# Kernel tuning notes

Measured on AMD Instinct MI355X. Metric: run time of the kernel, lower is better.

Reference implementation:

```python
import jax, jax.numpy as jnp
import numpy as np

B, T, D = 2, 1024, 1024
H, DK, DV = 16, 64, 128   # head_dim=64, head_v_dim=128 (expand_v=2)
F_HID, CONV = 2816, 4
EPS = 1e-6


def rmsnorm(x, w, eps=EPS):
    return x * jax.lax.rsqrt(jnp.mean(x * x, -1, keepdims=True) + eps) * w


def l2norm(x, eps=1e-6):
    return x * jax.lax.rsqrt(jnp.sum(x * x, -1, keepdims=True) + eps)


def short_conv(x, w):
    # causal depthwise conv1d (kernel CONV, no bias) + silu; x: [B,T,C], w: [C,K]
    K = w.shape[1]
    xp = jnp.pad(x, ((0, 0), (K - 1, 0), (0, 0)))
    y = jax.lax.conv_general_dilated(
        xp, w.T[:, None, :], (1,), 'VALID',
        dimension_numbers=('NWC', 'WIO', 'NWC'), feature_group_count=w.shape[0])
    return jax.nn.silu(y)


def gated_delta_rule(q, k, v, g, beta):
    # q,k: [B,T,H,DK], v: [B,T,H,DV], g,beta: [B,T,H]
    scale = q.shape[-1] ** -0.5
    q = l2norm(q) * scale
    k = l2norm(k)

    def step(S, inp):
        qt, kt, vt, gt, bt = inp          # S: [B,H,DK,DV]
        S = S * jnp.exp(gt)[..., None, None]
        err = jnp.einsum('bhk,bhkv->bhv', kt, S)
        vt = (vt - err) * bt[..., None]
        S = S + kt[..., :, None] * vt[..., None, :]
        ot = jnp.einsum('bhk,bhkv->bhv', qt, S)
        return S, ot

    S0 = jnp.zeros((q.shape[0], H, DK, DV), q.dtype)
    inputs = tuple(jnp.moveaxis(a, 1, 0) for a in (q, k, v, g, beta))
    _, o = jax.lax.scan(step, S0, inputs)
    return jnp.moveaxis(o, 0, 1)  # [B,T,H,DV]


def setup_inputs():
    key = jax.random.key(0)
    ks = jax.random.split(key, 20)
    w = lambda k, shape, s=0.02: jax.random.normal(k, shape, jnp.float32) * s
    return {
        'x': jax.random.normal(ks[0], (B, T, D), jnp.float32),
        'norm1_w': jnp.ones((D,), jnp.float32),
        'norm2_w': jnp.ones((D,), jnp.float32),
        'Wq': w(ks[1], (D, H * DK)),
        'Wk': w(ks[2], (D, H * DK)),
        'Wv': w(ks[3], (D, H * DV)),
        'conv_q': w(ks[4], (H * DK, CONV), 0.3),
        'conv_k': w(ks[5], (H * DK, CONV), 0.3),
        'conv_v': w(ks[6], (H * DV, CONV), 0.3),
        'Wa': w(ks[7], (D, H)),
        'Wb': w(ks[8], (D, H)),
        'dt_bias': jnp.log(jnp.expm1(jax.random.uniform(ks[9], (H,), minval=0.001, maxval=0.1))),
        'A_log': jnp.log(jax.random.uniform(ks[10], (H,), minval=1.0, maxval=16.0)),
        'Wg': w(ks[11], (D, H * DV)),
        'o_norm_w': jnp.ones((DV,), jnp.float32),
        'Wo': w(ks[12], (H * DV, D)),
        'W1': w(ks[13], (D, F_HID)),
        'W3': w(ks[14], (D, F_HID)),
        'W2': w(ks[15], (F_HID, D)),
    }


def reference(x, norm1_w, norm2_w, Wq, Wk, Wv, conv_q, conv_k, conv_v,
              Wa, Wb, dt_bias, A_log, Wg, o_norm_w, Wo, W1, W3, W2):
    # --- pre-norm + GatedDeltaNet ---
    h = rmsnorm(x, norm1_w)
    q = short_conv(h @ Wq, conv_q).reshape(B, T, H, DK)
    k = short_conv(h @ Wk, conv_k).reshape(B, T, H, DK)
    v = short_conv(h @ Wv, conv_v).reshape(B, T, H, DV)
    beta = jax.nn.sigmoid(h @ Wb)                                  # [B,T,H]
    g = -jnp.exp(A_log) * jax.nn.softplus(h @ Wa + dt_bias)       # [B,T,H] decay log
    o = gated_delta_rule(q, k, v, g, beta)                         # [B,T,H,DV]
    gate = (h @ Wg).reshape(B, T, H, DV)
    o = rmsnorm(o, o_norm_w, 1e-5) * jax.nn.silu(gate)             # gated RMSNorm
    x = x + o.reshape(B, T, H * DV) @ Wo                           # residual 1
    # --- pre-norm + SwiGLU FFN ---
    h2 = rmsnorm(x, norm2_w)
    ffn = (jax.nn.silu(h2 @ W1) * (h2 @ W3)) @ W2
    return x + ffn
```

## Files before the change

kernel.cpp:

```cpp
#include <hip/hip_runtime.h>
#include <hip/hip_bf16.h>
#include <math.h>

#define B_  2
#define T_  1024
#define D_  1024
#define H_  16
#define DK_ 64
#define DV_ 128
#define FH_ 2816
#define M_  (B_ * T_)
#define C_  64
#define NCH (T_ / C_)

typedef __attribute__((ext_vector_type(8))) short bf16x8;
typedef __attribute__((ext_vector_type(4))) float f32x4;

__global__ __launch_bounds__(256) void rmsnorm_k(
    const float* __restrict__ x, const float* __restrict__ w,
    float* __restrict__ outf, __hip_bfloat16* __restrict__ outb,
    int D, float eps) {
  const int row = blockIdx.x;
  const float* xr = x + (size_t)row * D;
  float ss = 0.f;
  for (int i = threadIdx.x; i < D; i += blockDim.x) { float v = xr[i]; ss += v * v; }
  for (int off = 32; off > 0; off >>= 1) ss += __shfl_xor(ss, off, 64);
  __shared__ float wsum[4];
  __shared__ float s_scale;
  const int lane = threadIdx.x & 63, wid = threadIdx.x >> 6;
  if (lane == 0) wsum[wid] = ss;
  __syncthreads();
  if (threadIdx.x == 0) {
    float tot = 0.f;
    const int nw = blockDim.x >> 6;
    for (int i = 0; i < nw; ++i) tot += wsum[i];
    s_scale = rsqrtf(tot / (float)D + eps);
  }
  __syncthreads();
  const float sc = s_scale;
  for (int i = threadIdx.x; i < D; i += blockDim.x) {
    const float v = xr[i] * sc * w[i];
    if (outf) outf[(size_t)row * D + i] = v;
    if (outb) outb[(size_t)row * D + i] = __float2bfloat16(v);
  }
}

__global__ __launch_bounds__(256) void transpose_bf16_k(
    const float* __restrict__ W, __hip_bfloat16* __restrict__ Wt, int K, int N) {
  __shared__ float t[32][33];
  const int k0 = blockIdx.y * 32, n0 = blockIdx.x * 32;
  const int c = threadIdx.x & 31, r = threadIdx.x >> 5;
#pragma unroll
  for (int i = 0; i < 4; ++i)
    t[r + 8 * i][c] = W[(size_t)(k0 + r + 8 * i) * N + n0 + c];
  __syncthreads();
#pragma unroll
  for (int i = 0; i < 4; ++i)
    Wt[(size_t)(n0 + r + 8 * i) * K + k0 + c] = __float2bfloat16(t[c][r + 8 * i]);
}

__device__ __forceinline__ void gload_lds16(const void* g, void* l) {
  __builtin_amdgcn_global_load_lds(
      (const __attribute__((address_space(1))) void*)g,
      (__attribute__((address_space(3))) void*)l, 16, 0, 0);
}

template<int BM, int BN>
__global__ __launch_bounds__(256) void mfma_gemm_k(
    const __hip_bfloat16* __restrict__ A, const __hip_bfloat16* __restrict__ Bt,
    const float* __restrict__ res, void* __restrict__ Cout,
    int M, int N, int K, int mode) {
  __shared__ __hip_bfloat16 As[2][BM * 32];
  __shared__ __hip_bfloat16 Bs[2][BN * 32];
  constexpr int MF = BM / 32;
  constexpr int NF = BN / 32;
  const int tid = threadIdx.x;
  const int lane = tid & 63;
  const int wv = tid >> 6;
  const int wm = (wv >> 1) * (BM / 2), wn = (wv & 1) * (BN / 2);
  const int bm = blockIdx.y * BM, bn = blockIdx.x * BN;
  const int l15 = lane & 15, lq8 = (lane >> 4) * 8;
  const int ar = tid >> 2;
  const int ac = (tid & 3) * 8;
  const size_t Abase = (size_t)(bm + ar) * K + ac;
  const size_t Bbase = (size_t)(bn + ar) * K + ac;
  f32x4 acc[MF][NF];
#pragma unroll
  for (int i = 0; i < MF; ++i)
#pragma unroll
    for (int j = 0; j < NF; ++j) acc[i][j] = (f32x4){0.f, 0.f, 0.f, 0.f};

  auto stage = [&](int buf, int k0) {
    gload_lds16(A + Abase + k0, (char*)&As[buf][0] + tid * 16);
    if constexpr (BM == 128)
      gload_lds16(A + Abase + (size_t)64 * K + k0,
                  (char*)&As[buf][0] + tid * 16 + 4096);
    gload_lds16(Bt + Bbase + k0, (char*)&Bs[buf][0] + tid * 16);
    if constexpr (BN == 128)
      gload_lds16(Bt + Bbase + (size_t)64 * K + k0,
                  (char*)&Bs[buf][0] + tid * 16 + 4096);
  };

  stage(0, 0);
  __syncthreads();
  int cur = 0;
#pragma unroll 2
  for (int k0 = 0; k0 < K; k0 += 32) {
    if (k0 + 32 < K) stage(cur ^ 1, k0 + 32);
    bf16x8 af[MF], bfr[NF];
#pragma unroll
    for (int i = 0; i < MF; ++i)
      af[i] = *(const bf16x8*)(&As[cur][0] + (wm + i * 16 + l15) * 32 + lq8);
#pragma unroll
    for (int j = 0; j < NF; ++j)
      bfr[j] = *(const bf16x8*)(&Bs[cur][0] + (wn + j * 16 + l15) * 32 + lq8);
#pragma unroll
    for (int i = 0; i < MF; ++i)
#pragma unroll
      for (int j = 0; j < NF; ++j)
        acc[i][j] = __builtin_amdgcn_mfma_f32_16x16x32_bf16(af[i], bfr[j], acc[i][j], 0, 0, 0);
    __syncthreads();
    cur ^= 1;
  }
  const int r0 = (lane >> 4) * 4;
#pragma unroll
  for (int i = 0; i < MF; ++i) {
#pragma unroll
    for (int j = 0; j < NF; ++j) {
      const int row = bm + wm + i * 16 + r0;
      const int col = bn + wn + j * 16 + l15;
#pragma unroll
      for (int r = 0; r < 4; ++r) {
        const size_t idx = (size_t)(row + r) * N + col;
        const float a = acc[i][j][r];
        if (mode == 0) ((float*)Cout)[idx] = a;
        else if (mode == 1) ((float*)Cout)[idx] = a + res[idx];
        else {
          const float s = res[idx];
          ((__hip_bfloat16*)Cout)[idx] =
              __float2bfloat16(s * (1.f / (1.f + __expf(-s))) * a);
        }
      }
    }
  }
}

__global__ __launch_bounds__(256) void skinny_k(
    const float* __restrict__ h, const float* __restrict__ Wa,
    const float* __restrict__ Wb, float* __restrict__ pa,
    float* __restrict__ pb, int K) {
  __shared__ float hl[D_];
  __shared__ float red[8][32];
  const int row = blockIdx.x;
  const int tid = threadIdx.x;
  {
    const float4* src = (const float4*)(h + (size_t)row * K);
    ((float4*)hl)[tid] = src[tid];
  }
  __syncthreads();
  const int col = tid & 31, sub = tid >> 5;
  const float* W = (col < 16) ? Wa : Wb;
  const int cc = col & 15;
  float s = 0.f;
  const int kk0 = sub * 128;
  for (int k = kk0; k < kk0 + 128; ++k) s += hl[k] * W[k * H_ + cc];
  red[sub][col] = s;
  __syncthreads();
  if (tid < 32) {
    float t = 0.f;
#pragma unroll
    for (int i = 0; i < 8; ++i) t += red[i][tid];
    if (tid < 16) pa[(size_t)row * H_ + tid] = t;
    else          pb[(size_t)row * H_ + tid - 16] = t;
  }
}

__global__ __launch_bounds__(256) void conv_silu_k(
    const float* __restrict__ src, const float* __restrict__ w,
    float* __restrict__ dst, int C, int sstr, int soff) {
  const int bt = blockIdx.x;
  const int b = bt / T_, t = bt % T_;
  const float* s = src + (size_t)b * T_ * sstr + soff;
  for (int c = threadIdx.x; c < C; c += blockDim.x) {
    const float w0 = w[c * 4 + 0], w1 = w[c * 4 + 1],
                w2 = w[c * 4 + 2], w3 = w[c * 4 + 3];
    float acc = s[(size_t)t * sstr + c] * w3;
    if (t >= 1) acc += s[(size_t)(t - 1) * sstr + c] * w2;
    if (t >= 2) acc += s[(size_t)(t - 2) * sstr + c] * w1;
    if (t >= 3) acc += s[(size_t)(t - 3) * sstr + c] * w0;
    dst[(size_t)bt * C + c] = acc * (1.f / (1.f + __expf(-acc)));
  }
}

__global__ void beta_g_k(const float* __restrict__ pa, const float* __restrict__ pb,
                         const float* __restrict__ dtb, const float* __restrict__ Alog,
                         float* __restrict__ g, float* __restrict__ beta, int n) {
  const int i = blockIdx.x * blockDim.x + threadIdx.x;
  if (i >= n) return;
  const int h = i & (H_ - 1);
  const float xx = pa[i] + dtb[h];
  const float sp = (xx > 20.f) ? xx : log1pf(expf(xx));
  g[i] = -expf(Alog[h]) * sp;
  beta[i] = 1.f / (1.f + expf(-pb[i]));
}

__global__ __launch_bounds__(64) void l2norm_k(float* __restrict__ q, float scale) {
  const size_t row = blockIdx.x;
  const int lane = threadIdx.x;
  const float v = q[row * 64 + lane];
  float ss = v * v;
  for (int off = 32; off > 0; off >>= 1) ss += __shfl_xor(ss, off, 64);
  q[row * 64 + lane] = v * rsqrtf(ss + 1e-6f) * scale;
}

__global__ __launch_bounds__(256) void chunk_prep_k(
    const float* __restrict__ q, float* __restrict__ k, float* __restrict__ v,
    const float* __restrict__ g, const float* __restrict__ beta,
    float* __restrict__ qkd, float* __restrict__ kdt, float* __restrict__ gam,
    float* __restrict__ wt) {
  const int task = blockIdx.x;
  const int bh = task >> 4, n = task & (NCH - 1);
  const int b = bh >> 4, h = bh & 15;
  const int t0 = n * C_;
  const int tid = threadIdx.x;
  __shared__ float lk[C_][68];
  __shared__ float Gs[C_][68];
  __shared__ float Xs[C_][100];
  __shared__ float Td[4][16][17];
  __shared__ float lb[C_], lgam[C_], lbeta[C_], lbg[C_];
  {
    const int r = tid >> 2, cq = (tid & 3) * 16;
    const float* src = k + (((size_t)b * T_ + t0 + r) * H_ + h) * DK_ + cq;
#pragma unroll
    for (int i = 0; i < 4; ++i)
      *(float4*)&lk[r][cq + 4 * i] = ((const float4*)src)[i];
  }
  if (tid < 64) {
    const size_t gi = ((size_t)b * T_ + t0 + tid) * H_ + h;
    float xx = g[gi];
    const float bb = beta[gi];
    lbeta[tid] = bb;
#pragma unroll
    for (int off = 1; off < 64; off <<= 1) {
      float y = __shfl_up(xx, off, 64);
      if (tid >= off) xx += y;
    }
    lb[tid] = xx;
    const float gm = __expf(xx);
    lgam[tid] = gm;
    lbg[tid] = bb * gm;
  }
  __syncthreads();
  const int r4g = (tid >> 4) * 4;
  const int sl = tid & 15;
  {
    const float* qg = q + (((size_t)b * T_ + t0) * H_ + h) * DK_;
    float accA[4][4] = {};
    float accQ[4][4] = {};
    for (int d = 0; d < 64; d += 4) {
      float4 kt[4], ks[4], qt[4];
#pragma unroll
      for (int i = 0; i < 4; ++i) kt[i] = *(const float4*)&lk[r4g + i][d];
#pragma unroll
      for (int j = 0; j < 4; ++j) ks[j] = *(const float4*)&lk[sl + 16 * j][d];
#pragma unroll
      for (int i = 0; i < 4; ++i) qt[i] = *(const float4*)(qg + (size_t)(r4g + i) * (H_ * DK_) + d);
#pragma unroll
      for (int i = 0; i < 4; ++i)
#pragma unroll
        for (int j = 0; j < 4; ++j) {
          accA[i][j] += kt[i].x * ks[j].x + kt[i].y * ks[j].y + kt[i].z * ks[j].z + kt[i].w * ks[j].w;
          accQ[i][j] += qt[i].x * ks[j].x + qt[i].y * ks[j].y + qt[i].z * ks[j].z + qt[i].w * ks[j].w;
        }
    }
    float* qo = qkd + (size_t)task * 4096;
#pragma unroll
    for (int i = 0; i < 4; ++i)
#pragma unroll
      for (int j = 0; j < 4; ++j) {
        const int t = r4g + i, s = sl + 16 * j;
        const float dec = (s <= t) ? __expf(lb[t] - lb[s]) : 0.f;
        Gs[t][s] = (t > s) ? lbeta[t] * accA[i][j] * dec : 0.f;
        qo[t * 64 + s] = accQ[i][j] * dec;
      }
  }
  {
    const int s = tid >> 2, dq = (tid & 3) * 16;
    const float e = __expf(lb[63] - lb[s]);
    float* dst = kdt + (size_t)task * 4096 + s * 64 + dq;
#pragma unroll
    for (int m = 0; m < 4; ++m) {
      float4 kv = *(const float4*)&lk[s][dq + 4 * m];
      kv.x *= e; kv.y *= e; kv.z *= e; kv.w *= e;
      *(float4*)(dst + 4 * m) = kv;
    }
  }
  if (tid < 64) gam[(size_t)task * 64 + tid] = lgam[tid];
  __syncthreads();
  if (tid < 64) {
    const int blk = tid >> 4, cI = tid & 15;
    float Xc[16];
#pragma unroll
    for (int t = 0; t < 16; ++t) Xc[t] = (t == cI) ? 1.f : 0.f;
#pragma unroll
    for (int t = 1; t < 16; ++t) {
      float acc = 0.f;
#pragma unroll
      for (int s = 0; s < t; ++s)
        acc += Gs[blk * 16 + t][blk * 16 + s] * Xc[s];
      Xc[t] -= acc;
    }
#pragma unroll
    for (int t = 0; t < 16; ++t) Td[blk][t][cI] = Xc[t];
  } else {
    for (int idx = tid - 64; idx < 64 * 96; idx += 192) {
      const int t = idx / 96, c = idx % 96;
      Xs[t][c] = lbeta[t] * v[(((size_t)b * T_ + t0 + t) * H_ + h) * DV_ + c];
    }
  }
  __syncthreads();
  const int rt = tid & 15;
  const int cg = tid >> 4;
#pragma unroll 1
  for (int half = 0; half < 2; ++half) {
#pragma unroll
    for (int bi = 0; bi < 4; ++bi) {
      if (bi > 0) {
        float acc[6] = {0.f, 0.f, 0.f, 0.f, 0.f, 0.f};
        for (int kk = 0; kk < 16 * bi; ++kk) {
          const float gvv = Gs[16 * bi + rt][kk];
#pragma unroll
          for (int c = 0; c < 6; ++c) acc[c] += gvv * Xs[kk][cg * 6 + c];
        }
#pragma unroll
        for (int c = 0; c < 6; ++c) Xs[16 * bi + rt][cg * 6 + c] -= acc[c];
      }
      float y[6] = {0.f, 0.f, 0.f, 0.f, 0.f, 0.f};
#pragma unroll
      for (int s = 0; s < 16; ++s) {
        const float tv = Td[bi][rt][s];
#pragma unroll
        for (int c = 0; c < 6; ++c) y[c] += tv * Xs[16 * bi + s][cg * 6 + c];
      }
#pragma unroll
      for (int c = 0; c < 6; ++c) Xs[16 * bi + rt][cg * 6 + c] = y[c];
    }
    __syncthreads();
    if (half == 0) {
      for (int idx = tid; idx < 64 * 96; idx += 256) {
        const int t = idx / 96, c = idx % 96;
        v[(((size_t)b * T_ + t0 + t) * H_ + h) * DV_ + c] = Xs[t][c];
      }
      __syncthreads();
      for (int idx = tid; idx < 64 * 96; idx += 256) {
        const int t = idx / 96, c = idx % 96;
        if (c < 32)
          Xs[t][c] = lbeta[t] * v[(((size_t)b * T_ + t0 + t) * H_ + h) * DV_ + 96 + c];
        else
          Xs[t][c] = lbg[t] * lk[t][c - 32];
      }
      __syncthreads();
    } else {
      for (int idx = tid; idx < 64 * 32; idx += 256) {
        const int t = idx >> 5, cc = idx & 31;
        v[(((size_t)b * T_ + t0 + t) * H_ + h) * DV_ + 96 + cc] = Xs[t][cc];
      }
      {
        const int dk = tid & 63, tg = tid >> 6;
        float buf[16];
#pragma unroll
        for (int j = 0; j < 16; ++j) buf[j] = Xs[16 * tg + j][32 + dk];
        float* dst = wt + (size_t)task * 4096 + dk * 64 + 16 * tg;
#pragma unroll
        for (int m = 0; m < 4; ++m)
          *(float4*)(dst + 4 * m) =
              make_float4(buf[4 * m], buf[4 * m + 1], buf[4 * m + 2], buf[4 * m + 3]);
      }
    }
  }
}

__global__ __launch_bounds__(256) void chunk_rec_k(
    const float* __restrict__ WT, float* __restrict__ u,
    const float* __restrict__ kdtT, const float* __restrict__ gam,
    float* __restrict__ Sst) {
  const int bh = blockIdx.x & 31, cg = blockIdx.x >> 5;
  const int b = bh >> 4, h = bh & 15;
  const int c0 = cg * 16;
  const int tid = threadIdx.x;
  const int w = tid >> 6;
  const int lane = tid & 63;
  const int L15 = lane & 15;
  const int t4 = L15 * 4;
  const int c = w * 4 + (lane >> 4);
  const int iot = tid >> 2;
  const int ioq = (tid & 3) * 4;

  __shared__ float Wt[2][64 * 64];
  __shared__ float Kt[2][64 * 64];
  __shared__ float SsT[16][68];
  __shared__ float UbT[16][68];
  __shared__ float Ub0[64][17];

  float Sr[4];
#pragma unroll
  for (int i = 0; i < 4; ++i) Sr[i] = 0.f;
#pragma unroll
  for (int i = 0; i < 4; ++i) SsT[c][t4 + i] = 0.f;

  {
    const float* sW = WT + (size_t)(bh * NCH) * 4096 + w * 1024 + lane * 4;
    const float* sK = kdtT + (size_t)(bh * NCH) * 4096 + w * 1024 + lane * 4;
    char* lW = (char*)&Wt[0][w * 1024] + lane * 16;
    char* lK = (char*)&Kt[0][w * 1024] + lane * 16;
#pragma unroll
    for (int i = 0; i < 4; ++i) {
      gload_lds16(sW + i * 256, lW + i * 1024);
      gload_lds16(sK + i * 256, lK + i * 1024);
    }
  }
  __syncthreads();

#pragma unroll 1
  for (int n = 0; n < NCH; ++n) {
    const int cur = n & 1, nx = cur ^ 1;
    const int task = bh * NCH + n;
    const int t0 = n * C_;
    const int n1 = (n + 1 < NCH) ? n + 1 : NCH - 1;
    const int task1 = bh * NCH + n1;
    const float gC = gam[(size_t)task * 64 + 63];

    const float4 uv = *(const float4*)(
        u + (((size_t)b * T_ + t0 + iot) * H_ + h) * DV_ + c0 + ioq);
    {
      const float* sW = WT + (size_t)task1 * 4096 + w * 1024 + lane * 4;
      const float* sK = kdtT + (size_t)task1 * 4096 + w * 1024 + lane * 4;
      char* lW = (char*)&Wt[nx][w * 1024] + lane * 16;
      char* lK = (char*)&Kt[nx][w * 1024] + lane * 16;
#pragma unroll
      for (int i = 0; i < 4; ++i) {
        gload_lds16(sW + i * 256, lW + i * 1024);
        gload_lds16(sK + i * 256, lK + i * 1024);
      }
    }
    __builtin_amdgcn_sched_barrier(0);
    {
      float4 sv;
      sv.x = SsT[ioq + 0][iot]; sv.y = SsT[ioq + 1][iot];
      sv.z = SsT[ioq + 2][iot]; sv.w = SsT[ioq + 3][iot];
      *(float4*)(Sst + (size_t)task * 8192 + iot * 128 + c0 + ioq) = sv;
    }
    float4 srow[16];
#pragma unroll
    for (int g = 0; g < 16; ++g) srow[g] = *(const float4*)&SsT[c][4 * g];
    float acc[4] = {0.f, 0.f, 0.f, 0.f};
#pragma unroll
    for (int g = 0; g < 16; ++g) {
      const float sj[4] = {srow[g].x, srow[g].y, srow[g].z, srow[g].w};
#pragma unroll
      for (int j = 0; j < 4; ++j) {
        const float4 wv = *(const float4*)&Wt[cur][(4 * g + j) * 64 + t4];
        acc[0] += wv.x * sj[j]; acc[1] += wv.y * sj[j];
        acc[2] += wv.z * sj[j]; acc[3] += wv.w * sj[j];
      }
    }
    Ub0[iot][ioq + 0] = uv.x; Ub0[iot][ioq + 1] = uv.y;
    Ub0[iot][ioq + 2] = uv.z; Ub0[iot][ioq + 3] = uv.w;
    __syncthreads();

#pragma unroll
    for (int i = 0; i < 4; ++i)
      UbT[c][t4 + i] = Ub0[t4 + i][c] - acc[i];
    float4 urow[16];
#pragma unroll
    for (int g = 0; g < 16; ++g) urow[g] = *(const float4*)&UbT[c][4 * g];
    float ac2[4] = {0.f, 0.f, 0.f, 0.f};
#pragma unroll
    for (int g = 0; g < 16; ++g) {
      const float uj[4] = {urow[g].x, urow[g].y, urow[g].z, urow[g].w};
#pragma unroll
      for (int j = 0; j < 4; ++j) {
        const float4 kv = *(const float4*)&Kt[cur][(4 * g + j) * 64 + t4];
        ac2[0] += kv.x * uj[j]; ac2[1] += kv.y * uj[j];
        ac2[2] += kv.z * uj[j]; ac2[3] += kv.w * uj[j];
      }
    }
#pragma unroll
    for (int i = 0; i < 4; ++i) {
      Sr[i] = gC * Sr[i] + ac2[i];
      SsT[c][t4 + i] = Sr[i];
    }
    __syncthreads();

    {
      float4 ov;
      ov.x = UbT[ioq + 0][iot]; ov.y = UbT[ioq + 1][iot];
      ov.z = UbT[ioq + 2][iot]; ov.w = UbT[ioq + 3][iot];
      *(float4*)(u + (((size_t)b * T_ + t0 + iot) * H_ + h) * DV_ + c0 + ioq) = ov;
    }
  }
}

__global__ __launch_bounds__(128) void chunk_o_k(
    const float* __restrict__ q, const float* __restrict__ qkd,
    const float* __restrict__ ub, const float* __restrict__ Sst,
    const float* __restrict__ gam, const float* __restrict__ gate,
    const float* __restrict__ onw, __hip_bfloat16* __restrict__ go) {
  const int task = blockIdx.x;
  const int bh = task >> 4, n = task & 15;
  const int b = bh >> 4, h = bh & 15;
  const int t0 = n * C_;
  const int tid = threadIdx.x;
  const int rowg = tid >> 4, colg = tid & 15;
  const int r8 = rowg * 8, c4 = colg * 4;
  __shared__ float At[64][68];
  __shared__ float Bs[64][132];
  __shared__ float lgam[64];
  if (tid < 64) lgam[tid] = gam[(size_t)task * 64 + tid];
  __syncthreads();
  const int t2 = tid >> 1, dh = (tid & 1) * 32;
  {
    const float* src = q + (((size_t)b * T_ + t0 + t2) * H_ + h) * DK_ + dh;
    const float sc = lgam[t2];
#pragma unroll
    for (int i = 0; i < 8; ++i) {
      const float4 v = ((const float4*)src)[i];
      At[dh + 4 * i + 0][t2] = v.x * sc; At[dh + 4 * i + 1][t2] = v.y * sc;
      At[dh + 4 * i + 2][t2] = v.z * sc; At[dh + 4 * i + 3][t2] = v.w * sc;
    }
  }
  {
    const float* src = Sst + (size_t)task * 8192 + t2 * 128 + (tid & 1) * 64;
    float* dst = &Bs[t2][(tid & 1) * 64];
#pragma unroll
    for (int i = 0; i < 16; ++i) ((float4*)dst)[i] = ((const float4*)src)[i];
  }
  __syncthreads();
  float acc[8][8];
#pragma unroll
  for (int i = 0; i < 8; ++i)
#pragma unroll
    for (int c = 0; c < 8; ++c) acc[i][c] = 0.f;
#pragma unroll 1
  for (int ph = 0; ph < 2; ++ph) {
    for (int kb = 0; kb < 64; kb += 4) {
#pragma unroll
      for (int j = 0; j < 4; ++j) {
        const float4 alo = *(const float4*)&At[kb + j][r8];
        const float4 ahi = *(const float4*)&At[kb + j][r8 + 4];
        const float4 blo = *(const float4*)&Bs[kb + j][c4];
        const float4 bhi = *(const float4*)&Bs[kb + j][c4 + 64];
        const float av[8] = {alo.x, alo.y, alo.z, alo.w, ahi.x, ahi.y, ahi.z, ahi.w};
        const float bv[8] = {blo.x, blo.y, blo.z, blo.w, bhi.x, bhi.y, bhi.z, bhi.w};
#pragma unroll
        for (int i = 0; i < 8; ++i)
#pragma unroll
          for (int c = 0; c < 8; ++c) acc[i][c] += av[i] * bv[c];
      }
    }
    if (ph == 0) {
      __syncthreads();
      {
        const float* src = qkd + (size_t)task * 4096 + t2 * 64 + dh;
#pragma unroll
        for (int i = 0; i < 8; ++i) {
          const float4 v = ((const float4*)src)[i];
          At[dh + 4 * i + 0][t2] = v.x; At[dh + 4 * i + 1][t2] = v.y;
          At[dh + 4 * i + 2][t2] = v.z; At[dh + 4 * i + 3][t2] = v.w;
        }
      }
      {
        const float* src = ub + (((size_t)b * T_ + t0 + t2) * H_ + h) * DV_ + (tid & 1) * 64;
        float* dst = &Bs[t2][(tid & 1) * 64];
#pragma unroll
        for (int i = 0; i < 16; ++i) ((float4*)dst)[i] = ((const float4*)src)[i];
      }
      __syncthreads();
    }
  }
#pragma unroll
  for (int i = 0; i < 8; ++i) {
    float pr = 0.f;
#pragma unroll
    for (int c = 0; c < 8; ++c) pr += acc[i][c] * acc[i][c];
    pr += __shfl_xor(pr, 1, 64);
    pr += __shfl_xor(pr, 2, 64);
    pr += __shfl_xor(pr, 4, 64);
    pr += __shfl_xor(pr, 8, 64);
    const float rms = rsqrtf(pr / (float)DV_ + 1e-5f);
    const size_t rb = (((size_t)b * T_ + t0 + r8 + i) * H_ + h) * DV_;
    const float4 glo = *(const float4*)(gate + rb + c4);
    const float4 ghi = *(const float4*)(gate + rb + c4 + 64);
    const float gv[8] = {glo.x, glo.y, glo.z, glo.w, ghi.x, ghi.y, ghi.z, ghi.w};
    unsigned short outv[8];
#pragma unroll
    for (int c = 0; c < 8; ++c) {
      const int col = (c < 4) ? c4 + c : c4 + 60 + c;
      const float gg = gv[c];
      const float val = acc[i][c] * rms * onw[col] * gg * (1.f / (1.f + __expf(-gg)));
      const __hip_bfloat16 bfv = __float2bfloat16(val);
      outv[c] = *(const unsigned short*)&bfv;
    }
    *(ushort4*)((unsigned short*)go + rb + c4) =
        make_ushort4(outv[0], outv[1], outv[2], outv[3]);
    *(ushort4*)((unsigned short*)go + rb + c4 + 64) =
        make_ushort4(outv[4], outv[5], outv[6], outv[7]);
  }
}

extern "C" void kernel_launch(void* const* d_in, const int* in_sizes, int n_in,
                              void* d_out, int out_size, void* d_ws, size_t ws_size,
                              hipStream_t stream) {
  const float* x    = (const float*)d_in[0];
  const float* n1w  = (const float*)d_in[1];
  const float* n2w  = (const float*)d_in[2];
  const float* Wq   = (const float*)d_in[3];
  const float* Wk   = (const float*)d_in[4];
  const float* Wv   = (const float*)d_in[5];
  const float* cq   = (const float*)d_in[6];
  const float* ck   = (const float*)d_in[7];
  const float* cv   = (const float*)d_in[8];
  const float* Wa   = (const float*)d_in[9];
  const float* Wb   = (const float*)d_in[10];
  const float* dtb  = (const float*)d_in[11];
  const float* Alog = (const float*)d_in[12];
  const float* Wg   = (const float*)d_in[13];
  const float* onw  = (const float*)d_in[14];
  const float* Wo   = (const float*)d_in[15];
  const float* W1   = (const float*)d_in[16];
  const float* W3   = (const float*)d_in[17];
  const float* W2   = (const float*)d_in[18];
  float* out = (float*)d_out;
  float* ws  = (float*)d_ws;

  const size_t SZ_MD = (size_t)M_ * D_;
  const size_t SZ_MV = (size_t)M_ * H_ * DV_;
  float* h    = ws;
  float* pq   = ws + SZ_MD;
  float* pk   = ws + 2 * SZ_MD;
  float* pv   = ws + 3 * SZ_MD;
  float* gate = ws + 3 * SZ_MD + SZ_MV;
  float* qb   = ws + 3 * SZ_MD + 2 * SZ_MV;
  float* kb   = ws + 4 * SZ_MD + 2 * SZ_MV;
  float* vb   = ws + 5 * SZ_MD + 2 * SZ_MV;
  float* Sst  = pv;
  float* y1   = pq;
  float* a1   = pv;
  float* wtb  = h;
  float* qk   = pq;
  float* smalls = ws + 5 * SZ_MD + 3 * SZ_MV;
  float* pa  = smalls;
  float* pb  = pa + (size_t)M_ * H_;
  float* gv  = pb + (size_t)M_ * H_;
  float* bv  = gv + (size_t)M_ * H_;
  float* gam = bv + (size_t)M_ * H_;
  __hip_bfloat16* h_bf  = (__hip_bfloat16*)vb;
  __hip_bfloat16* wb1   = (__hip_bfloat16*)kb;
  __hip_bfloat16* wb2   = (__hip_bfloat16*)vb;
  __hip_bfloat16* go_bf = (__hip_bfloat16*)h;
  __hip_bfloat16* h2_bf = (__hip_bfloat16*)h;
  __hip_bfloat16* a1b   = (__hip_bfloat16*)qb;

  const dim3 blk256(256);
  const dim3 g_tr1024_1024(1024 / 32, 1024 / 32);
  const dim3 g_tr1024_2048(2048 / 32, 1024 / 32);
  const dim3 g_tr2048_1024(1024 / 32, 2048 / 32);
  const dim3 g_tr1024_2816(2816 / 32, 1024 / 32);
  const dim3 g_tr2816_1024(1024 / 32, 2816 / 32);

  rmsnorm_k<<<dim3(M_), blk256, 0, stream>>>(x, n1w, h, h_bf, D_, 1e-6f);
  transpose_bf16_k<<<g_tr1024_1024, blk256, 0, stream>>>(Wq, wb1, D_, 1024);
  transpose_bf16_k<<<g_tr1024_1024, blk256, 0, stream>>>(Wk, wb1 + (size_t)1024 * 1024, D_, 1024);
  mfma_gemm_k<128, 64><<<dim3(2048 / 64, M_ / 128), blk256, 0, stream>>>(h_bf, wb1, nullptr, qk, M_, 2048, D_, 0);
  transpose_bf16_k<<<g_tr1024_2048, blk256, 0, stream>>>(Wv, wb1, D_, 2048);
  mfma_gemm_k<128, 64><<<dim3(2048 / 64, M_ / 128), blk256, 0, stream>>>(h_bf, wb1, nullptr, pv, M_, 2048, D_, 0);
  transpose_bf16_k<<<g_tr1024_2048, blk256, 0, stream>>>(Wg, wb1, D_, 2048);
  mfma_gemm_k<128, 64><<<dim3(2048 / 64, M_ / 128), blk256, 0, stream>>>(h_bf, wb1, nullptr, gate, M_, 2048, D_, 0);
  skinny_k<<<dim3(M_), blk256, 0, stream>>>(h, Wa, Wb, pa, pb, D_);
  conv_silu_k<<<dim3(M_), blk256, 0, stream>>>(qk, cq, qb, H_ * DK_, 2048, 0);
  conv_silu_k<<<dim3(M_), blk256, 0, stream>>>(qk, ck, kb, H_ * DK_, 2048, 1024);
  conv_silu_k<<<dim3(M_), blk256, 0, stream>>>(pv, cv, vb, H_ * DV_, 2048, 0);
  beta_g_k<<<dim3((M_ * H_ + 255) / 256), blk256, 0, stream>>>(pa, pb, dtb, Alog, gv, bv, M_ * H_);
  l2norm_k<<<dim3(M_ * H_), dim3(64), 0, stream>>>(qb, 0.125f);
  l2norm_k<<<dim3(M_ * H_), dim3(64), 0, stream>>>(kb, 1.0f);
  chunk_prep_k<<<dim3(32 * NCH), blk256, 0, stream>>>(qb, kb, vb, gv, bv, pq, pk, gam, wtb);
  chunk_rec_k<<<dim3(256), blk256, 0, stream>>>(wtb, vb, pk, gam, Sst);
  chunk_o_k<<<dim3(32 * NCH), dim3(128), 0, stream>>>(qb, pq, vb, Sst, gam, gate, onw, go_bf);
  transpose_bf16_k<<<g_tr2048_1024, blk256, 0, stream>>>(Wo, wb2, H_ * DV_, 1024);
  mfma_gemm_k<64, 64><<<dim3(1024 / 64, M_ / 64), blk256, 0, stream>>>(go_bf, wb2, x, y1, M_, 1024, H_ * DV_, 1);
  rmsnorm_k<<<dim3(M_), blk256, 0, stream>>>(y1, n2w, nullptr, h2_bf, D_, 1e-6f);
  transpose_bf16_k<<<g_tr1024_2816, blk256, 0, stream>>>(W1, wb2, D_, FH_);
  mfma_gemm_k<128, 64><<<dim3(FH_ / 64, M_ / 128), blk256, 0, stream>>>(h2_bf, wb2, nullptr, a1, M_, FH_, D_, 0);
  transpose_bf16_k<<<g_tr1024_2816, blk256, 0, stream>>>(W3, wb2, D_, FH_);
  mfma_gemm_k<128, 64><<<dim3(FH_ / 64, M_ / 128), blk256, 0, stream>>>(h2_bf, wb2, a1, a1b, M_, FH_, D_, 2);
  transpose_bf16_k<<<g_tr2816_1024, blk256, 0, stream>>>(W2, wb2, FH_, 1024);
  mfma_gemm_k<64, 64><<<dim3(1024 / 64, M_ / 64), blk256, 0, stream>>>(a1b, wb2, y1, out, M_, 1024, FH_, 1);
}
```

Before: 580.8 us.

## Widen chunk recurrence to 512 threads and merge Q/K/V projection GEMMs

The chunk recurrence kernel now runs 512 threads per block. Each thread owns 2 state columns instead of 4, which halves the per-thread serial FMA chain in the latency-bound inter-chunk loop; the tile loads are re-indexed to match. Separately, the Wv transpose is written next to Wq/Wk so that a single 4096-wide GEMM produces q, k and v, and the conv kernels read from the merged buffer with stride 4096. The trade-off is more LDS traffic per FMA and larger barrier cost from more waves per block, in exchange for one fewer GEMM launch and better occupancy of that GEMM.

```diff
diff --git a/kernel.cpp b/kernel.cpp
--- a/kernel.cpp
+++ b/kernel.cpp
@@ -380,7 +380,7 @@
   }
 }
 
-__global__ __launch_bounds__(256) void chunk_rec_k(
+__global__ __launch_bounds__(512) void chunk_rec_k(
     const float* __restrict__ WT, float* __restrict__ u,
     const float* __restrict__ kdtT, const float* __restrict__ gam,
     float* __restrict__ Sst) {
@@ -390,11 +390,10 @@
   const int tid = threadIdx.x;
   const int w = tid >> 6;
   const int lane = tid & 63;
-  const int L15 = lane & 15;
-  const int t4 = L15 * 4;
-  const int c = w * 4 + (lane >> 4);
-  const int iot = tid >> 2;
-  const int ioq = (tid & 3) * 4;
+  const int t2 = (lane & 31) * 2;
+  const int c = w * 2 + (lane >> 5);
+  const int iot = tid >> 3;
+  const int ioq = (tid & 7) * 2;
 
   __shared__ float Wt[2][64 * 64];
   __shared__ float Kt[2][64 * 64];
@@ -402,22 +401,17 @@
   __shared__ float UbT[16][68];
   __shared__ float Ub0[64][17];
 
-  float Sr[4];
-#pragma unroll
-  for (int i = 0; i < 4; ++i) Sr[i] = 0.f;
-#pragma unroll
-  for (int i = 0; i < 4; ++i) SsT[c][t4 + i] = 0.f;
+  float Sr0 = 0.f, Sr1 = 0.f;
+  SsT[c][t2] = 0.f;
+  SsT[c][t2 + 1] = 0.f;
 
   {
-    const float* sW = WT + (size_t)(bh * NCH) * 4096 + w * 1024 + lane * 4;
-    const float* sK = kdtT + (size_t)(bh * NCH) * 4096 + w * 1024 + lane * 4;
-    char* lW = (char*)&Wt[0][w * 1024] + lane * 16;
-    char* lK = (char*)&Kt[0][w * 1024] + lane * 16;
-#pragma unroll
-    for (int i = 0; i < 4; ++i) {
-      gload_lds16(sW + i * 256, lW + i * 1024);
-      gload_lds16(sK + i * 256, lK + i * 1024);
-    }
+    const float* sW = WT + (size_t)(bh * NCH) * 4096 + tid * 4;
+    const float* sK = kdtT + (size_t)(bh * NCH) * 4096 + tid * 4;
+    gload_lds16(sW, (char*)&Wt[0][0] + tid * 16);
+    gload_lds16(sW + 2048, (char*)&Wt[0][2048] + tid * 16);
+    gload_lds16(sK, (char*)&Kt[0][0] + tid * 16);
+    gload_lds16(sK + 2048, (char*)&Kt[0][2048] + tid * 16);
   }
   __syncthreads();
 
@@ -430,73 +424,70 @@
     const int task1 = bh * NCH + n1;
     const float gC = gam[(size_t)task * 64 + 63];
 
-    const float4 uv = *(const float4*)(
+    const float2 uv = *(const float2*)(
         u + (((size_t)b * T_ + t0 + iot) * H_ + h) * DV_ + c0 + ioq);
     {
-      const float* sW = WT + (size_t)task1 * 4096 + w * 1024 + lane * 4;
-      const float* sK = kdtT + (size_t)task1 * 4096 + w * 1024 + lane * 4;
-      char* lW = (char*)&Wt[nx][w * 1024] + lane * 16;
-      char* lK = (char*)&Kt[nx][w * 1024] + lane * 16;
-#pragma unroll
-      for (int i = 0; i < 4; ++i) {
-        gload_lds16(sW + i * 256, lW + i * 1024);
-        gload_lds16(sK + i * 256, lK + i * 1024);
-      }
+      const float* sW = WT + (size_t)task1 * 4096 + tid * 4;
+      const float* sK = kdtT + (size_t)task1 * 4096 + tid * 4;
+      gload_lds16(sW, (char*)&Wt[nx][0] + tid * 16);
+      gload_lds16(sW + 2048, (char*)&Wt[nx][2048] + tid * 16);
+      gload_lds16(sK, (char*)&Kt[nx][0] + tid * 16);
+      gload_lds16(sK + 2048, (char*)&Kt[nx][2048] + tid * 16);
     }
     __builtin_amdgcn_sched_barrier(0);
     {
-      float4 sv;
-      sv.x = SsT[ioq + 0][iot]; sv.y = SsT[ioq + 1][iot];
-      sv.z = SsT[ioq + 2][iot]; sv.w = SsT[ioq + 3][iot];
-      *(float4*)(Sst + (size_t)task * 8192 + iot * 128 + c0 + ioq) = sv;
+      float2 sv;
+      sv.x = SsT[ioq + 0][iot];
+      sv.y = SsT[ioq + 1][iot];
+      *(float2*)(Sst + (size_t)task * 8192 + iot * 128 + c0 + ioq) = sv;
     }
     float4 srow[16];
 #pragma unroll
     for (int g = 0; g < 16; ++g) srow[g] = *(const float4*)&SsT[c][4 * g];
-    float acc[4] = {0.f, 0.f, 0.f, 0.f};
+    float a0 = 0.f, a1 = 0.f;
 #pragma unroll
     for (int g = 0; g < 16; ++g) {
       const float sj[4] = {srow[g].x, srow[g].y, srow[g].z, srow[g].w};
 #pragma unroll
       for (int j = 0; j < 4; ++j) {
-        const float4 wv = *(const float4*)&Wt[cur][(4 * g + j) * 64 + t4];
-        acc[0] += wv.x * sj[j]; acc[1] += wv.y * sj[j];
-        acc[2] += wv.z * sj[j]; acc[3] += wv.w * sj[j];
-      }
-    }
-    Ub0[iot][ioq + 0] = uv.x; Ub0[iot][ioq + 1] = uv.y;
-    Ub0[iot][ioq + 2] = uv.z; Ub0[iot][ioq + 3] = uv.w;
+        const float2 wv = *(const float2*)&Wt[cur][(4 * g + j) * 64 + t2];
+        a0 += wv.x * sj[j];
+        a1 += wv.y * sj[j];
+      }
+    }
+    Ub0[iot][ioq + 0] = uv.x;
+    Ub0[iot][ioq + 1] = uv.y;
     __syncthreads();
 
-#pragma unroll
-    for (int i = 0; i < 4; ++i)
-      UbT[c][t4 + i] = Ub0[t4 + i][c] - acc[i];
+    const float u0 = Ub0[t2 + 0][c] - a0;
+    const float u1 = Ub0[t2 + 1][c] - a1;
+    UbT[c][t2 + 0] = u0;
+    UbT[c][t2 + 1] = u1;
     float4 urow[16];
 #pragma unroll
     for (int g = 0; g < 16; ++g) urow[g] = *(const float4*)&UbT[c][4 * g];
-    float ac2[4] = {0.f, 0.f, 0.f, 0.f};
+    float b0 = 0.f, b1 = 0.f;
 #pragma unroll
     for (int g = 0; g < 16; ++g) {
       const float uj[4] = {urow[g].x, urow[g].y, urow[g].z, urow[g].w};
 #pragma unroll
       for (int j = 0; j < 4; ++j) {
-        const float4 kv = *(const float4*)&Kt[cur][(4 * g + j) * 64 + t4];
-        ac2[0] += kv.x * uj[j]; ac2[1] += kv.y * uj[j];
-        ac2[2] += kv.z * uj[j]; ac2[3] += kv.w * uj[j];
-      }
-    }
-#pragma unroll
-    for (int i = 0; i < 4; ++i) {
-      Sr[i] = gC * Sr[i] + ac2[i];
-      SsT[c][t4 + i] = Sr[i];
-    }
+        const float2 kv = *(const float2*)&Kt[cur][(4 * g + j) * 64 + t2];
+        b0 += kv.x * uj[j];
+        b1 += kv.y * uj[j];
+      }
+    }
+    Sr0 = gC * Sr0 + b0;
+    Sr1 = gC * Sr1 + b1;
+    SsT[c][t2 + 0] = Sr0;
+    SsT[c][t2 + 1] = Sr1;
     __syncthreads();
 
     {
-      float4 ov;
-      ov.x = UbT[ioq + 0][iot]; ov.y = UbT[ioq + 1][iot];
-      ov.z = UbT[ioq + 2][iot]; ov.w = UbT[ioq + 3][iot];
-      *(float4*)(u + (((size_t)b * T_ + t0 + iot) * H_ + h) * DV_ + c0 + ioq) = ov;
+      float2 ov;
+      ov.x = UbT[ioq + 0][iot];
+      ov.y = UbT[ioq + 1][iot];
+      *(float2*)(u + (((size_t)b * T_ + t0 + iot) * H_ + h) * DV_ + c0 + ioq) = ov;
     }
   }
 }
@@ -647,7 +638,7 @@
   float* y1   = pq;
   float* a1   = pv;
   float* wtb  = h;
-  float* qk   = pq;
+  float* proj = pq;
   float* smalls = ws + 5 * SZ_MD + 3 * SZ_MV;
   float* pa  = smalls;
   float* pb  = pa + (size_t)M_ * H_;
@@ -671,20 +662,19 @@
   rmsnorm_k<<<dim3(M_), blk256, 0, stream>>>(x, n1w, h, h_bf, D_, 1e-6f);
   transpose_bf16_k<<<g_tr1024_1024, blk256, 0, stream>>>(Wq, wb1, D_, 1024);
   transpose_bf16_k<<<g_tr1024_1024, blk256, 0, stream>>>(Wk, wb1 + (size_t)1024 * 1024, D_, 1024);
-  mfma_gemm_k<128, 64><<<dim3(2048 / 64, M_ / 128), blk256, 0, stream>>>(h_bf, wb1, nullptr, qk, M_, 2048, D_, 0);
-  transpose_bf16_k<<<g_tr1024_2048, blk256, 0, stream>>>(Wv, wb1, D_, 2048);
-  mfma_gemm_k<128, 64><<<dim3(2048 / 64, M_ / 128), blk256, 0, stream>>>(h_bf, wb1, nullptr, pv, M_, 2048, D_, 0);
+  transpose_bf16_k<<<g_tr1024_2048, blk256, 0, stream>>>(Wv, wb1 + (size_t)2048 * 1024, D_, 2048);
+  mfma_gemm_k<128, 64><<<dim3(4096 / 64, M_ / 128), blk256, 0, stream>>>(h_bf, wb1, nullptr, proj, M_, 4096, D_, 0);
   transpose_bf16_k<<<g_tr1024_2048, blk256, 0, stream>>>(Wg, wb1, D_, 2048);
   mfma_gemm_k<128, 64><<<dim3(2048 / 64, M_ / 128), blk256, 0, stream>>>(h_bf, wb1, nullptr, gate, M_, 2048, D_, 0);
   skinny_k<<<dim3(M_), blk256, 0, stream>>>(h, Wa, Wb, pa, pb, D_);
-  conv_silu_k<<<dim3(M_), blk256, 0, stream>>>(qk, cq, qb, H_ * DK_, 2048, 0);
-  conv_silu_k<<<dim3(M_), blk256, 0, stream>>>(qk, ck, kb, H_ * DK_, 2048, 1024);
-  conv_silu_k<<<dim3(M_), blk256, 0, stream>>>(pv, cv, vb, H_ * DV_, 2048, 0);
+  conv_silu_k<<<dim3(M_), blk256, 0, stream>>>(proj, cq, qb, H_ * DK_, 4096, 0);
+  conv_silu_k<<<dim3(M_), blk256, 0, stream>>>(proj, ck, kb, H_ * DK_, 4096, 1024);
+  conv_silu_k<<<dim3(M_), blk256, 0, stream>>>(proj, cv, vb, H_ * DV_, 4096, 2048);
   beta_g_k<<<dim3((M_ * H_ + 255) / 256), blk256, 0, stream>>>(pa, pb, dtb, Alog, gv, bv, M_ * H_);
   l2norm_k<<<dim3(M_ * H_), dim3(64), 0, stream>>>(qb, 0.125f);
   l2norm_k<<<dim3(M_ * H_), dim3(64), 0, stream>>>(kb, 1.0f);
   chunk_prep_k<<<dim3(32 * NCH), blk256, 0, stream>>>(qb, kb, vb, gv, bv, pq, pk, gam, wtb);
-  chunk_rec_k<<<dim3(256), blk256, 0, stream>>>(wtb, vb, pk, gam, Sst);
+  chunk_rec_k<<<dim3(256), dim3(512), 0, stream>>>(wtb, vb, pk, gam, Sst);
   chunk_o_k<<<dim3(32 * NCH), dim3(128), 0, stream>>>(qb, pq, vb, Sst, gam, gate, onw, go_bf);
   transpose_bf16_k<<<g_tr2048_1024, blk256, 0, stream>>>(Wo, wb2, H_ * DV_, 1024);
   mfma_gemm_k<64, 64><<<dim3(1024 / 64, M_ / 64), blk256, 0, stream>>>(go_bf, wb2, x, y1, M_, 1024, H_ * DV_, 1);
```

Result: no change. 575.1 us (-1.0%).
